# Optimization experiments

Measured on AMD Instinct MI355X. Metric: run time of the kernel, lower is better.

## Reference

```python
import jax, jax.numpy as jnp
import numpy as np

DIM = 1024
NUM_HEADS = 16
HEAD_DIM = DIM // NUM_HEADS
SCALE = HEAD_DIM ** -0.5
NEG = -1e9


def setup_inputs() -> dict:
    key = jax.random.key(0)
    ks = jax.random.split(key, 10)
    B, N, M, C = 8, 1024, 1024, DIM
    q = jax.random.normal(ks[0], (B, N, C), jnp.float32)
    k = jax.random.normal(ks[1], (B, M, C), jnp.float32)
    v = jax.random.normal(ks[2], (B, M, C), jnp.float32)
    mask = jax.random.randint(ks[3], (B, N), 0, 2, jnp.int32)
    target_mask = jax.random.randint(ks[4], (B, N, M), 0, 2, jnp.int32)
    Wq = jax.random.normal(ks[5], (C, C), jnp.float32) * 0.02
    Wk = jax.random.normal(ks[6], (C, C), jnp.float32) * 0.02
    Wv = jax.random.normal(ks[7], (C, C), jnp.float32) * 0.02
    Wo = jax.random.normal(ks[8], (C, C), jnp.float32) * 0.02
    bo = jnp.zeros((C,), jnp.float32)
    return {"q": q, "k": k, "v": v, "mask": mask, "target_mask": target_mask,
            "Wq": Wq, "Wk": Wk, "Wv": Wv, "Wo": Wo, "bo": bo}


def reference(q, k, v, mask, target_mask, Wq, Wk, Wv, Wo, bo):
    B, N, C = q.shape
    M = k.shape[1]
    H, D = NUM_HEADS, HEAD_DIM
    qh = (q @ Wq).reshape(B, N, H, D)
    kh = (k @ Wk).reshape(B, M, H, D)
    vh = (v @ Wv).reshape(B, M, H, D)
    attn = jnp.einsum('bnhd,bmhd->bhnm', qh, kh) * SCALE  # (B,H,N,M)
    # self-attn key mask (B,N) -> broadcast over queries (requires N==M as in original)
    attn = jnp.where(mask[:, None, None, :] == 0, NEG, attn)
    # cross-attn mask (B,N,M) -> broadcast over heads
    attn = jnp.where(target_mask[:, None, :, :] == 0, NEG, attn)
    attn = jax.nn.softmax(attn, axis=-1)
    x = jnp.einsum('bhnm,bmhd->bnhd', attn, vh).reshape(B, N, C)
    return x @ Wo + bo
```

## Files before the change

kernel.cpp:

```cpp
#include <hip/hip_runtime.h>
#include <hip/hip_bf16.h>

#define DEV __device__ __forceinline__

typedef __attribute__((ext_vector_type(8))) short bf16x8;
typedef __attribute__((ext_vector_type(4))) float f32x4;
typedef unsigned int u32;
typedef unsigned long long u64;

DEV short f2bf(float f) {
  union { float f; u32 u; } x; x.f = f;
  u32 r = x.u + 0x7fffu + ((x.u >> 16) & 1u);
  return (short)(r >> 16);
}

DEV void gload_lds16(const void* g, void* l) {
  __builtin_amdgcn_global_load_lds(
      (const __attribute__((address_space(1))) u32*)g,
      (__attribute__((address_space(3))) u32*)l, 16, 0, 0);
}

DEV void stage_t128(const char* base, int ktb, char* lds, int w, int lane) {
  int r8 = lane >> 3;
  int csw = ((lane & 7) ^ r8) << 4;
#pragma unroll
  for (int i = 0; i < 4; ++i) {
    int c = w * 4 + i;
    gload_lds16(base + (size_t)(c * 8 + r8) * 2048 + ktb + csw, lds + c * 1024);
  }
}

DEV bf16x8 frag(const short* L, int row, int col) {
  return *(const bf16x8*)&L[row * 64 + (col ^ ((row & 7) << 3))];
}

__global__ __launch_bounds__(256) void aconv(const float* __restrict__ q,
    const float* __restrict__ k, const float* __restrict__ v,
    short* __restrict__ qb, short* __restrict__ kb, short* __restrict__ vb) {
  const float* src; short* dst;
  if (blockIdx.z == 0)      { src = q; dst = qb; }
  else if (blockIdx.z == 1) { src = k; dst = kb; }
  else                      { src = v; dst = vb; }
  size_t i = ((size_t)blockIdx.x * 256 + threadIdx.x) * 8;
  float4 f0 = *(const float4*)(src + i);
  float4 f1 = *(const float4*)(src + i + 4);
  bf16x8 o;
  o[0] = f2bf(f0.x); o[1] = f2bf(f0.y); o[2] = f2bf(f0.z); o[3] = f2bf(f0.w);
  o[4] = f2bf(f1.x); o[5] = f2bf(f1.y); o[6] = f2bf(f1.z); o[7] = f2bf(f1.w);
  *(bf16x8*)(dst + i) = o;
}

__global__ __launch_bounds__(256) void pack_mask(const int* __restrict__ mask,
                                                 const int* __restrict__ tmask,
                                                 u64* __restrict__ pk) {
  int bn = blockIdx.x;
  int b = bn >> 10;
  int t = threadIdx.x, w = t >> 6, lane = t & 63;
  const int* tr = tmask + (size_t)bn * 1024;
  const int* mr = mask + b * 1024;
#pragma unroll
  for (int it = 0; it < 4; ++it) {
    int m = it * 256 + w * 64 + lane;
    bool on = (mr[m] != 0) && (tr[m] != 0);
    u64 bits = __ballot(on);
    if (lane == 0) pk[(size_t)bn * 16 + it * 4 + w] = bits;
  }
}

__global__ __launch_bounds__(256) void wconv4(const float* __restrict__ W0,
    const float* __restrict__ W1, const float* __restrict__ W2,
    const float* __restrict__ W3, short* __restrict__ WtAll) {
  const float* W = blockIdx.z == 0 ? W0 : blockIdx.z == 1 ? W1
                 : blockIdx.z == 2 ? W2 : W3;
  short* Wt = WtAll + (size_t)blockIdx.z * 1024 * 1024;
  __shared__ short tile[64][65];
  int k0 = blockIdx.x * 64, n0 = blockIdx.y * 64;
  int t = threadIdx.x;
  int r = t >> 2, c = (t & 3) * 16;
  const float* src = W + (size_t)(k0 + r) * 1024 + n0 + c;
#pragma unroll
  for (int i = 0; i < 16; i += 4) {
    float4 f = *(const float4*)(src + i);
    tile[r][c + i + 0] = f2bf(f.x);
    tile[r][c + i + 1] = f2bf(f.y);
    tile[r][c + i + 2] = f2bf(f.z);
    tile[r][c + i + 3] = f2bf(f.w);
  }
  __syncthreads();
  bf16x8 v0, v1;
#pragma unroll
  for (int i = 0; i < 8; ++i) v0[i] = tile[c + i][r];
#pragma unroll
  for (int i = 0; i < 8; ++i) v1[i] = tile[c + 8 + i][r];
  short* dst = Wt + (size_t)(n0 + r) * 1024 + k0 + c;
  *(bf16x8*)(dst) = v0;
  *(bf16x8*)(dst + 8) = v1;
}

__global__ __launch_bounds__(256) void vtrans(const short* __restrict__ vh,
                                              short* __restrict__ vht) {
  __shared__ short tile[64][65];
  int m0 = blockIdx.x * 64;
  int bh = blockIdx.y;
  int t = threadIdx.x;
  int r = t >> 2, c = (t & 3) * 16;
  const short* src = vh + ((size_t)bh * 1024 + m0 + r) * 64 + c;
  bf16x8 a0 = *(const bf16x8*)(src);
  bf16x8 a1 = *(const bf16x8*)(src + 8);
#pragma unroll
  for (int i = 0; i < 8; ++i) tile[r][c + i] = a0[i];
#pragma unroll
  for (int i = 0; i < 8; ++i) tile[r][c + 8 + i] = a1[i];
  __syncthreads();
  bf16x8 v0, v1;
#pragma unroll
  for (int i = 0; i < 8; ++i) v0[i] = tile[c + i][r];
#pragma unroll
  for (int i = 0; i < 8; ++i) v1[i] = tile[c + 8 + i][r];
  short* dst = vht + ((size_t)bh * 64 + r) * 1024 + m0 + c;
  *(bf16x8*)dst = v0;
  *(bf16x8*)(dst + 8) = v1;
}

#define QSCALE 0.18033688011112042f

__global__ __launch_bounds__(256, 2) void gemm_qkv(
    const short* __restrict__ qb, const short* __restrict__ kb, const short* __restrict__ vb,
    const short* __restrict__ WtAll,
    short* __restrict__ qh, short* __restrict__ kh, short* __restrict__ vh) {
  int flat = blockIdx.z * 512 + blockIdx.y * 8 + blockIdx.x;
  int nid = (flat & 7) * 192 + (flat >> 3);
  int zz = nid >> 9;
  int rr = nid & 511;
  int bm = (rr >> 3) * 128, bn = (rr & 7) * 128;

  const short* A; short* Ch; float cs;
  if (zz == 0)      { A = qb; Ch = qh; cs = QSCALE; }
  else if (zz == 1) { A = kb; Ch = kh; cs = 1.0f; }
  else              { A = vb; Ch = vh; cs = 1.0f; }
  const short* Wt = WtAll + (size_t)zz * 1024 * 1024;

  __shared__ __align__(16) short As[128 * 64];
  __shared__ __align__(16) short Bs[128 * 64];

  int tid = threadIdx.x;
  int lane = tid & 63, w = tid >> 6;
  int wm = w >> 1, wn = w & 1;
  int lr = lane & 15, lg = lane >> 4;

  const f32x4 fz = {0.f, 0.f, 0.f, 0.f};
  f32x4 acc[4][4];
#pragma unroll
  for (int i = 0; i < 4; ++i)
#pragma unroll
    for (int j = 0; j < 4; ++j) acc[i][j] = fz;

  const char* abase = (const char*)A + (size_t)bm * 2048;
  const char* bbase = (const char*)Wt + (size_t)bn * 2048;

  for (int ktb = 0; ktb < 2048; ktb += 128) {
    stage_t128(abase, ktb, (char*)As, w, lane);
    stage_t128(bbase, ktb, (char*)Bs, w, lane);
    __syncthreads();
#pragma unroll
    for (int ks = 0; ks < 2; ++ks) {
      bf16x8 af[4], bfr[4];
#pragma unroll
      for (int mi = 0; mi < 4; ++mi)
        af[mi] = frag(As, wm * 64 + mi * 16 + lr, ks * 32 + lg * 8);
#pragma unroll
      for (int ni = 0; ni < 4; ++ni)
        bfr[ni] = frag(Bs, wn * 64 + ni * 16 + lr, ks * 32 + lg * 8);
#pragma unroll
      for (int mi = 0; mi < 4; ++mi)
#pragma unroll
        for (int ni = 0; ni < 4; ++ni)
          acc[mi][ni] = __builtin_amdgcn_mfma_f32_16x16x32_bf16(af[mi], bfr[ni], acc[mi][ni], 0, 0, 0);
    }
    __syncthreads();
  }
#pragma unroll
  for (int mi = 0; mi < 4; ++mi)
#pragma unroll
    for (int ni = 0; ni < 4; ++ni) {
      int ccol = bn + wn * 64 + ni * 16 + lr;
      int h = ccol >> 6, d = ccol & 63;
#pragma unroll
      for (int j = 0; j < 4; ++j) {
        int r = bm + wm * 64 + mi * 16 + lg * 4 + j;
        int bb = r >> 10, n = r & 1023;
        Ch[(((size_t)bb * 16 + h) * 1024 + n) * 64 + d] = f2bf(acc[mi][ni][j] * cs);
      }
    }
}

DEV void stage_kv(const char* kbase, const char* vbase, int kv0,
                  short* Ksb, short* Vsb, int w, int lane) {
#pragma unroll
  for (int i = 0; i < 2; ++i) {
    int c = w * 2 + i;
    int row = (lane >> 3);
    int colb = ((lane & 7) ^ row) << 4;
    gload_lds16(kbase + (size_t)(kv0 + c * 8 + row) * 128 + colb, (char*)Ksb + c * 1024);
    gload_lds16(vbase + (size_t)(c * 8 + row) * 2048 + kv0 * 2 + colb, (char*)Vsb + c * 1024);
  }
}

__global__ __launch_bounds__(256, 2) void attn(
    const short* __restrict__ qh, const short* __restrict__ kh, const short* __restrict__ vht,
    const u64* __restrict__ pk, short* __restrict__ x) {
  __shared__ __align__(16) short Ks[2][4096];
  __shared__ __align__(16) short Vs[2][4096];
  __shared__ __align__(16) short Ps[2][8192];

  int flat = blockIdx.y * 8 + blockIdx.x;
  int nid = (flat & 7) * 64 + (flat >> 3);
  int bh = nid >> 2, qp = nid & 3;
  int b = bh >> 4;
  int tid = threadIdx.x, lane = tid & 63, w = tid >> 6;
  int lr = lane & 15, lg = lane >> 4;

  bf16x8 qa[2][2][2];
#pragma unroll
  for (int sub = 0; sub < 2; ++sub) {
    const short* qb2 = qh + ((size_t)bh * 1024 + qp * 256 + sub * 128 + w * 32) * 64;
#pragma unroll
    for (int mi = 0; mi < 2; ++mi)
#pragma unroll
      for (int ks = 0; ks < 2; ++ks)
        qa[sub][mi][ks] = *(const bf16x8*)(qb2 + (mi * 16 + lr) * 64 + ks * 32 + lg * 8);
  }

  const f32x4 fz = {0.f, 0.f, 0.f, 0.f};
  f32x4 o[2][2][4];
  float psum[2][2][4];
#pragma unroll
  for (int sub = 0; sub < 2; ++sub)
#pragma unroll
    for (int mi = 0; mi < 2; ++mi)
#pragma unroll
      for (int j = 0; j < 4; ++j) { psum[sub][mi][j] = 0.f; o[sub][mi][j] = fz; }

  const char* kbase = (const char*)(kh + (size_t)bh * 65536);
  const char* vbase = (const char*)(vht + (size_t)bh * 65536);
  const u64* pkb = pk + ((size_t)b * 1024 + qp * 256) * 16;

  stage_kv(kbase, vbase, 0, Ks[0], Vs[0], w, lane);
  __syncthreads();
  int cur = 0;

  for (int t = 0; t < 16; ++t) {
    if (t < 15) stage_kv(kbase, vbase, (t + 1) * 64, Ks[cur ^ 1], Vs[cur ^ 1], w, lane);

#pragma unroll
    for (int sub = 0; sub < 2; ++sub) {
      u64 pw[2][4];
#pragma unroll
      for (int mi = 0; mi < 2; ++mi)
#pragma unroll
        for (int j = 0; j < 4; ++j)
          pw[mi][j] = pkb[(sub * 128 + w * 32 + mi * 16 + lg * 4 + j) * 16 + t];

      f32x4 s[2][4];
#pragma unroll
      for (int mi = 0; mi < 2; ++mi)
#pragma unroll
        for (int ni = 0; ni < 4; ++ni) s[mi][ni] = fz;
      __builtin_amdgcn_s_setprio(1);
#pragma unroll
      for (int ks = 0; ks < 2; ++ks) {
        bf16x8 kb2[4];
#pragma unroll
        for (int ni = 0; ni < 4; ++ni)
          kb2[ni] = *(const bf16x8*)&Ks[cur][(ni * 16 + lr) * 64 + ((ks * 32 + lg * 8) ^ ((lr & 7) << 3))];
#pragma unroll
        for (int mi = 0; mi < 2; ++mi)
#pragma unroll
          for (int ni = 0; ni < 4; ++ni)
            s[mi][ni] = __builtin_amdgcn_mfma_f32_16x16x32_bf16(qa[sub][mi][ks], kb2[ni], s[mi][ni], 0, 0, 0);
      }
      __builtin_amdgcn_s_setprio(0);

#pragma unroll
      for (int mi = 0; mi < 2; ++mi)
#pragma unroll
        for (int j = 0; j < 4; ++j) {
          u32 lo = (u32)pw[mi][j], hi = (u32)(pw[mi][j] >> 32);
          int r = w * 32 + mi * 16 + lg * 4 + j;
          int sw = (r & 7) << 3;
          float rs = 0.f;
#pragma unroll
          for (int ni = 0; ni < 4; ++ni) {
            u32 bit = ((ni < 2 ? lo : hi) >> ((ni & 1) * 16 + lr)) & 1u;
            float e = __builtin_amdgcn_exp2f(s[mi][ni][j]);
            float p = bit ? e : 0.f;
            rs += p;
            union { float f; u32 u; } cv; cv.f = p;
            Ps[sub][r * 64 + ((ni * 16 + lr) ^ sw)] = (short)((cv.u + 0x8000u) >> 16);
          }
          psum[sub][mi][j] += rs;
        }

      __builtin_amdgcn_s_setprio(1);
#pragma unroll
      for (int ks = 0; ks < 2; ++ks) {
        bf16x8 pa[2], vb2[4];
#pragma unroll
        for (int mi = 0; mi < 2; ++mi)
          pa[mi] = *(const bf16x8*)&Ps[sub][(w * 32 + mi * 16 + lr) * 64 + ((ks * 32 + lg * 8) ^ ((lr & 7) << 3))];
#pragma unroll
        for (int nd = 0; nd < 4; ++nd)
          vb2[nd] = *(const bf16x8*)&Vs[cur][(nd * 16 + lr) * 64 + ((ks * 32 + lg * 8) ^ ((lr & 7) << 3))];
#pragma unroll
        for (int mi = 0; mi < 2; ++mi)
#pragma unroll
          for (int nd = 0; nd < 4; ++nd)
            o[sub][mi][nd] = __builtin_amdgcn_mfma_f32_16x16x32_bf16(pa[mi], vb2[nd], o[sub][mi][nd], 0, 0, 0);
      }
      __builtin_amdgcn_s_setprio(0);
    }
    __syncthreads();
    cur ^= 1;
  }

  short* xb = x + ((size_t)b * 1024) * 1024 + (bh & 15) * 64;
#pragma unroll
  for (int sub = 0; sub < 2; ++sub)
#pragma unroll
    for (int mi = 0; mi < 2; ++mi)
#pragma unroll
      for (int j = 0; j < 4; ++j) {
        float rs = psum[sub][mi][j];
#pragma unroll
        for (int dd = 1; dd < 16; dd <<= 1) rs += __shfl_xor(rs, dd, 64);
        float inv = rs > 0.f ? 1.0f / rs : 0.f;
        int qg = qp * 256 + sub * 128 + w * 32 + mi * 16 + lg * 4 + j;
#pragma unroll
        for (int nd = 0; nd < 4; ++nd) {
          int d = nd * 16 + lr;
          xb[(size_t)qg * 1024 + d] = f2bf(o[sub][mi][nd][j] * inv);
        }
      }
}

__global__ __launch_bounds__(256, 2) void gemm_out(
    const short* __restrict__ X, const short* __restrict__ Wot,
    const float* __restrict__ bo, float* __restrict__ out) {
  int flat = blockIdx.y * 8 + blockIdx.x;
  int nid = (flat & 7) * 64 + (flat >> 3);
  int bm = (nid >> 3) * 128, bn = (nid & 7) * 128;

  __shared__ __align__(16) short As[128 * 64];
  __shared__ __align__(16) short Bs[128 * 64];
  int tid = threadIdx.x, lane = tid & 63, w = tid >> 6;
  int wm = w >> 1, wn = w & 1, lr = lane & 15, lg = lane >> 4;

  const f32x4 fz = {0.f, 0.f, 0.f, 0.f};
  f32x4 acc[4][4];
#pragma unroll
  for (int i = 0; i < 4; ++i)
#pragma unroll
    for (int j = 0; j < 4; ++j) acc[i][j] = fz;

  const char* abase = (const char*)X + (size_t)bm * 2048;
  const char* bbase = (const char*)Wot + (size_t)bn * 2048;

  for (int ktb = 0; ktb < 2048; ktb += 128) {
    stage_t128(abase, ktb, (char*)As, w, lane);
    stage_t128(bbase, ktb, (char*)Bs, w, lane);
    __syncthreads();
#pragma unroll
    for (int ks = 0; ks < 2; ++ks) {
      bf16x8 af[4], bfr[4];
#pragma unroll
      for (int mi = 0; mi < 4; ++mi)
        af[mi] = frag(As, wm * 64 + mi * 16 + lr, ks * 32 + lg * 8);
#pragma unroll
      for (int ni = 0; ni < 4; ++ni)
        bfr[ni] = frag(Bs, wn * 64 + ni * 16 + lr, ks * 32 + lg * 8);
#pragma unroll
      for (int mi = 0; mi < 4; ++mi)
#pragma unroll
        for (int ni = 0; ni < 4; ++ni)
          acc[mi][ni] = __builtin_amdgcn_mfma_f32_16x16x32_bf16(af[mi], bfr[ni], acc[mi][ni], 0, 0, 0);
    }
    __syncthreads();
  }
#pragma unroll
  for (int mi = 0; mi < 4; ++mi)
#pragma unroll
    for (int ni = 0; ni < 4; ++ni) {
      int ccol = bn + wn * 64 + ni * 16 + lr;
      float bias = bo[ccol];
#pragma unroll
      for (int j = 0; j < 4; ++j) {
        int r = bm + wm * 64 + mi * 16 + lg * 4 + j;
        out[(size_t)r * 1024 + ccol] = acc[mi][ni][j] + bias;
      }
    }
}

extern "C" void kernel_launch(void* const* d_in, const int* in_sizes, int n_in,
                              void* d_out, int out_size, void* d_ws, size_t ws_size,
                              hipStream_t stream) {
  const float* q = (const float*)d_in[0];
  const float* k = (const float*)d_in[1];
  const float* v = (const float*)d_in[2];
  const int* mask = (const int*)d_in[3];
  const int* tmask = (const int*)d_in[4];
  const float* Wq = (const float*)d_in[5];
  const float* Wk = (const float*)d_in[6];
  const float* Wv = (const float*)d_in[7];
  const float* Wo = (const float*)d_in[8];
  const float* bo = (const float*)d_in[9];
  float* out = (float*)d_out;

  char* ws = (char*)d_ws;
  const size_t MB = 1u << 20;
  if (ws_size < 73 * MB) return;
  short* WtAll = (short*)(ws + 0 * MB);
  short* qh  = (short*)(ws + 8 * MB);
  short* kh  = (short*)(ws + 24 * MB);
  short* vh  = (short*)(ws + 40 * MB);
  short* vht = (short*)(ws + 56 * MB);
  u64*   pkb = (u64*)(ws + 72 * MB);
  short* x   = (short*)(ws + 40 * MB);
  short* qbA = (short*)d_out;
  short* kbA = (short*)d_out + 8 * 1024 * 1024;
  short* vbA = (short*)(ws + 56 * MB);

  aconv<<<dim3(4096, 1, 3), 256, 0, stream>>>(q, k, v, qbA, kbA, vbA);
  wconv4<<<dim3(16, 16, 4), 256, 0, stream>>>(Wq, Wk, Wv, Wo, WtAll);
  pack_mask<<<dim3(8192), 256, 0, stream>>>(mask, tmask, pkb);

  gemm_qkv<<<dim3(8, 64, 3), 256, 0, stream>>>(qbA, kbA, vbA, WtAll, qh, kh, vh);
  vtrans<<<dim3(16, 128), 256, 0, stream>>>(vh, vht);
  attn<<<dim3(8, 64), 256, 0, stream>>>(qh, kh, vht, pkb, x);
  gemm_out<<<dim3(8, 64), 256, 0, stream>>>(x, WtAll + 3 * 1024 * 1024, bo, out);
}
```

Baseline: 335.9 us.

## Triple-buffer GEMMs with 256x128 tiles and merge prologue kernels

Result: slower. 356.4 us (+6.1%).

```diff
diff --git a/kernel.cpp b/kernel.cpp
--- a/kernel.cpp
+++ b/kernel.cpp
@@ -8,6 +8,8 @@
 typedef unsigned int u32;
 typedef unsigned long long u64;
 
+#define VMCNT(n) asm volatile("s_waitcnt vmcnt(" #n ")" ::: "memory")
+
 DEV short f2bf(float f) {
   union { float f; u32 u; } x; x.f = f;
   u32 r = x.u + 0x7fffu + ((x.u >> 16) & 1u);
@@ -20,81 +22,123 @@
       (__attribute__((address_space(3))) u32*)l, 16, 0, 0);
 }
 
-DEV void stage_t128(const char* base, int ktb, char* lds, int w, int lane) {
+DEV bf16x8 frag(const short* L, int row, int col) {
+  return *(const bf16x8*)&L[row * 64 + (col ^ ((row & 7) << 3))];
+}
+
+DEV void stageA256(const char* base, int ktb, char* lds, int w, int lane) {
   int r8 = lane >> 3;
   int csw = ((lane & 7) ^ r8) << 4;
 #pragma unroll
-  for (int i = 0; i < 4; ++i) {
-    int c = w * 4 + i;
+  for (int l = 0; l < 4; ++l) {
+    int c = l * 8 + w;
     gload_lds16(base + (size_t)(c * 8 + r8) * 2048 + ktb + csw, lds + c * 1024);
   }
 }
-
-DEV bf16x8 frag(const short* L, int row, int col) {
-  return *(const bf16x8*)&L[row * 64 + (col ^ ((row & 7) << 3))];
-}
-
-__global__ __launch_bounds__(256) void aconv(const float* __restrict__ q,
-    const float* __restrict__ k, const float* __restrict__ v,
-    short* __restrict__ qb, short* __restrict__ kb, short* __restrict__ vb) {
-  const float* src; short* dst;
-  if (blockIdx.z == 0)      { src = q; dst = qb; }
-  else if (blockIdx.z == 1) { src = k; dst = kb; }
-  else                      { src = v; dst = vb; }
-  size_t i = ((size_t)blockIdx.x * 256 + threadIdx.x) * 8;
-  float4 f0 = *(const float4*)(src + i);
-  float4 f1 = *(const float4*)(src + i + 4);
-  bf16x8 o;
-  o[0] = f2bf(f0.x); o[1] = f2bf(f0.y); o[2] = f2bf(f0.z); o[3] = f2bf(f0.w);
-  o[4] = f2bf(f1.x); o[5] = f2bf(f1.y); o[6] = f2bf(f1.z); o[7] = f2bf(f1.w);
-  *(bf16x8*)(dst + i) = o;
-}
-
-__global__ __launch_bounds__(256) void pack_mask(const int* __restrict__ mask,
-                                                 const int* __restrict__ tmask,
-                                                 u64* __restrict__ pk) {
-  int bn = blockIdx.x;
-  int b = bn >> 10;
-  int t = threadIdx.x, w = t >> 6, lane = t & 63;
-  const int* tr = tmask + (size_t)bn * 1024;
-  const int* mr = mask + b * 1024;
-#pragma unroll
-  for (int it = 0; it < 4; ++it) {
-    int m = it * 256 + w * 64 + lane;
-    bool on = (mr[m] != 0) && (tr[m] != 0);
-    u64 bits = __ballot(on);
-    if (lane == 0) pk[(size_t)bn * 16 + it * 4 + w] = bits;
-  }
-}
-
-__global__ __launch_bounds__(256) void wconv4(const float* __restrict__ W0,
-    const float* __restrict__ W1, const float* __restrict__ W2,
-    const float* __restrict__ W3, short* __restrict__ WtAll) {
-  const float* W = blockIdx.z == 0 ? W0 : blockIdx.z == 1 ? W1
-                 : blockIdx.z == 2 ? W2 : W3;
-  short* Wt = WtAll + (size_t)blockIdx.z * 1024 * 1024;
-  __shared__ short tile[64][65];
-  int k0 = blockIdx.x * 64, n0 = blockIdx.y * 64;
-  int t = threadIdx.x;
-  int r = t >> 2, c = (t & 3) * 16;
-  const float* src = W + (size_t)(k0 + r) * 1024 + n0 + c;
-#pragma unroll
-  for (int i = 0; i < 16; i += 4) {
-    float4 f = *(const float4*)(src + i);
-    tile[r][c + i + 0] = f2bf(f.x);
-    tile[r][c + i + 1] = f2bf(f.y);
-    tile[r][c + i + 2] = f2bf(f.z);
-    tile[r][c + i + 3] = f2bf(f.w);
-  }
-  __syncthreads();
-  bf16x8 v0, v1;
-#pragma unroll
-  for (int i = 0; i < 8; ++i) v0[i] = tile[c + i][r];
-#pragma unroll
-  for (int i = 0; i < 8; ++i) v1[i] = tile[c + 8 + i][r];
-  short* dst = Wt + (size_t)(n0 + r) * 1024 + k0 + c;
-  *(bf16x8*)(dst) = v0;
-  *(bf16x8*)(dst + 8) = v1;
+DEV void stageB128(const char* base, int ktb, char* lds, int w, int lane) {
+  int r8 = lane >> 3;
+  int csw = ((lane & 7) ^ r8) << 4;
+#pragma unroll
+  for (int l = 0; l < 2; ++l) {
+    int c = l * 8 + w;
+    gload_lds16(base + (size_t)(c * 8 + r8) * 2048 + ktb + csw, lds + c * 1024);
+  }
+}
+
+DEV void tile_compute(const short* Asb, const short* Bsb, f32x4 acc[8][2],
+                      int wm, int wn, int lr, int lg) {
+  bf16x8 bfrag[2][2];
+#pragma unroll
+  for (int ni = 0; ni < 2; ++ni)
+#pragma unroll
+    for (int ks = 0; ks < 2; ++ks)
+      bfrag[ni][ks] = frag(Bsb, wn * 32 + ni * 16 + lr, ks * 32 + lg * 8);
+#pragma unroll
+  for (int pi = 0; pi < 4; ++pi) {
+    bf16x8 af[2][2];
+#pragma unroll
+    for (int m2 = 0; m2 < 2; ++m2)
+#pragma unroll
+      for (int ks = 0; ks < 2; ++ks)
+        af[m2][ks] = frag(Asb, wm * 128 + (pi * 2 + m2) * 16 + lr, ks * 32 + lg * 8);
+    __builtin_amdgcn_s_setprio(1);
+#pragma unroll
+    for (int m2 = 0; m2 < 2; ++m2)
+#pragma unroll
+      for (int ni = 0; ni < 2; ++ni)
+#pragma unroll
+        for (int ks = 0; ks < 2; ++ks)
+          acc[pi * 2 + m2][ni] = __builtin_amdgcn_mfma_f32_16x16x32_bf16(
+              af[m2][ks], bfrag[ni][ks], acc[pi * 2 + m2][ni], 0, 0, 0);
+    __builtin_amdgcn_s_setprio(0);
+  }
+}
+
+#define ENTRY_SYNC()                          \
+  __builtin_amdgcn_sched_barrier(0);          \
+  __builtin_amdgcn_s_barrier();               \
+  __builtin_amdgcn_sched_barrier(0)
+
+__global__ __launch_bounds__(256) void prologue(
+    const float* __restrict__ q, const float* __restrict__ k, const float* __restrict__ v,
+    short* __restrict__ qb, short* __restrict__ kb, short* __restrict__ vb,
+    const float* __restrict__ W0, const float* __restrict__ W1,
+    const float* __restrict__ W2, const float* __restrict__ W3,
+    short* __restrict__ WtAll,
+    const int* __restrict__ mask, const int* __restrict__ tmask, u64* __restrict__ pk) {
+  int bx = blockIdx.x;
+  if (bx < 12288) {
+    int z = bx >> 12, bi = bx & 4095;
+    const float* src = z == 0 ? q : z == 1 ? k : v;
+    short* dst = z == 0 ? qb : z == 1 ? kb : vb;
+    size_t i = ((size_t)bi * 256 + threadIdx.x) * 8;
+    float4 f0 = *(const float4*)(src + i);
+    float4 f1 = *(const float4*)(src + i + 4);
+    bf16x8 o;
+    o[0] = f2bf(f0.x); o[1] = f2bf(f0.y); o[2] = f2bf(f0.z); o[3] = f2bf(f0.w);
+    o[4] = f2bf(f1.x); o[5] = f2bf(f1.y); o[6] = f2bf(f1.z); o[7] = f2bf(f1.w);
+    *(bf16x8*)(dst + i) = o;
+  } else if (bx < 13312) {
+    int idx = bx - 12288;
+    int z = idx >> 8, rem = idx & 255;
+    const float* W = z == 0 ? W0 : z == 1 ? W1 : z == 2 ? W2 : W3;
+    short* Wt = WtAll + (size_t)z * 1024 * 1024;
+    __shared__ short tile[64][65];
+    int k0 = (rem >> 4) * 64, n0 = (rem & 15) * 64;
+    int t = threadIdx.x;
+    int r = t >> 2, c = (t & 3) * 16;
+    const float* src = W + (size_t)(k0 + r) * 1024 + n0 + c;
+#pragma unroll
+    for (int i = 0; i < 16; i += 4) {
+      float4 f = *(const float4*)(src + i);
+      tile[r][c + i + 0] = f2bf(f.x);
+      tile[r][c + i + 1] = f2bf(f.y);
+      tile[r][c + i + 2] = f2bf(f.z);
+      tile[r][c + i + 3] = f2bf(f.w);
+    }
+    __syncthreads();
+    bf16x8 v0, v1;
+#pragma unroll
+    for (int i = 0; i < 8; ++i) v0[i] = tile[c + i][r];
+#pragma unroll
+    for (int i = 0; i < 8; ++i) v1[i] = tile[c + 8 + i][r];
+    short* dst = Wt + (size_t)(n0 + r) * 1024 + k0 + c;
+    *(bf16x8*)(dst) = v0;
+    *(bf16x8*)(dst + 8) = v1;
+  } else {
+    int bn = bx - 13312;
+    int b = bn >> 10;
+    int t = threadIdx.x, w = t >> 6, lane = t & 63;
+    const int* tr = tmask + (size_t)bn * 1024;
+    const int* mr = mask + b * 1024;
+#pragma unroll
+    for (int it = 0; it < 4; ++it) {
+      int m = it * 256 + w * 64 + lane;
+      bool on = (mr[m] != 0) && (tr[m] != 0);
+      u64 bits = __ballot(on);
+      if (lane == 0) pk[(size_t)bn * 16 + it * 4 + w] = bits;
+    }
+  }
 }
 
 __global__ __launch_bounds__(256) void vtrans(const short* __restrict__ vh,
@@ -124,15 +168,18 @@
 
 #define QSCALE 0.18033688011112042f
 
-__global__ __launch_bounds__(256, 2) void gemm_qkv(
+__global__ __launch_bounds__(512, 2) void gemm_qkv(
     const short* __restrict__ qb, const short* __restrict__ kb, const short* __restrict__ vb,
     const short* __restrict__ WtAll,
     short* __restrict__ qh, short* __restrict__ kh, short* __restrict__ vh) {
-  int flat = blockIdx.z * 512 + blockIdx.y * 8 + blockIdx.x;
-  int nid = (flat & 7) * 192 + (flat >> 3);
-  int zz = nid >> 9;
-  int rr = nid & 511;
-  int bm = (rr >> 3) * 128, bn = (rr & 7) * 128;
+  __shared__ __align__(16) short AsAll[3 * 256 * 64];
+  __shared__ __align__(16) short BsAll[3 * 128 * 64];
+
+  int flat = blockIdx.y * 8 + blockIdx.x;
+  int nid = (flat & 7) * 96 + (flat >> 3);
+  int zz = nid >> 8;
+  int rr = nid & 255;
+  int bm = (rr >> 3) * 256, bn = (rr & 7) * 128;
 
   const short* A; short* Ch; float cs;
   if (zz == 0)      { A = qb; Ch = qh; cs = QSCALE; }
@@ -140,56 +187,109 @@
   else              { A = vb; Ch = vh; cs = 1.0f; }
   const short* Wt = WtAll + (size_t)zz * 1024 * 1024;
 
-  __shared__ __align__(16) short As[128 * 64];
-  __shared__ __align__(16) short Bs[128 * 64];
-
   int tid = threadIdx.x;
   int lane = tid & 63, w = tid >> 6;
-  int wm = w >> 1, wn = w & 1;
+  int wm = w >> 2, wn = w & 3;
   int lr = lane & 15, lg = lane >> 4;
 
   const f32x4 fz = {0.f, 0.f, 0.f, 0.f};
-  f32x4 acc[4][4];
-#pragma unroll
-  for (int i = 0; i < 4; ++i)
-#pragma unroll
-    for (int j = 0; j < 4; ++j) acc[i][j] = fz;
+  f32x4 acc[8][2];
+#pragma unroll
+  for (int i = 0; i < 8; ++i) { acc[i][0] = fz; acc[i][1] = fz; }
 
   const char* abase = (const char*)A + (size_t)bm * 2048;
   const char* bbase = (const char*)Wt + (size_t)bn * 2048;
 
-  for (int ktb = 0; ktb < 2048; ktb += 128) {
-    stage_t128(abase, ktb, (char*)As, w, lane);
-    stage_t128(bbase, ktb, (char*)Bs, w, lane);
-    __syncthreads();
-#pragma unroll
-    for (int ks = 0; ks < 2; ++ks) {
-      bf16x8 af[4], bfr[4];
-#pragma unroll
-      for (int mi = 0; mi < 4; ++mi)
-        af[mi] = frag(As, wm * 64 + mi * 16 + lr, ks * 32 + lg * 8);
-#pragma unroll
-      for (int ni = 0; ni < 4; ++ni)
-        bfr[ni] = frag(Bs, wn * 64 + ni * 16 + lr, ks * 32 + lg * 8);
-#pragma unroll
-      for (int mi = 0; mi < 4; ++mi)
-#pragma unroll
-        for (int ni = 0; ni < 4; ++ni)
-          acc[mi][ni] = __builtin_amdgcn_mfma_f32_16x16x32_bf16(af[mi], bfr[ni], acc[mi][ni], 0, 0, 0);
-    }
-    __syncthreads();
-  }
-#pragma unroll
-  for (int mi = 0; mi < 4; ++mi)
-#pragma unroll
-    for (int ni = 0; ni < 4; ++ni) {
-      int ccol = bn + wn * 64 + ni * 16 + lr;
+  stageA256(abase, 0, (char*)AsAll, w, lane);
+  stageB128(bbase, 0, (char*)BsAll, w, lane);
+  stageA256(abase, 128, (char*)AsAll + 32768, w, lane);
+  stageB128(bbase, 128, (char*)BsAll + 16384, w, lane);
+
+  int cb = 0, sb = 2;
+  for (int t = 0; t < 15; ++t) {
+    VMCNT(6);
+    ENTRY_SYNC();
+    if (t < 14) {
+      stageA256(abase, (t + 2) * 128, (char*)AsAll + sb * 32768, w, lane);
+      stageB128(bbase, (t + 2) * 128, (char*)BsAll + sb * 16384, w, lane);
+    }
+    tile_compute(AsAll + cb * 16384, BsAll + cb * 8192, acc, wm, wn, lr, lg);
+    cb = (cb == 2) ? 0 : cb + 1;
+    sb = (sb == 2) ? 0 : sb + 1;
+  }
+  VMCNT(0);
+  ENTRY_SYNC();
+  tile_compute(AsAll + cb * 16384, BsAll + cb * 8192, acc, wm, wn, lr, lg);
+
+#pragma unroll
+  for (int mi = 0; mi < 8; ++mi)
+#pragma unroll
+    for (int ni = 0; ni < 2; ++ni) {
+      int ccol = bn + wn * 32 + ni * 16 + lr;
       int h = ccol >> 6, d = ccol & 63;
 #pragma unroll
       for (int j = 0; j < 4; ++j) {
-        int r = bm + wm * 64 + mi * 16 + lg * 4 + j;
+        int r = bm + wm * 128 + mi * 16 + lg * 4 + j;
         int bb = r >> 10, n = r & 1023;
         Ch[(((size_t)bb * 16 + h) * 1024 + n) * 64 + d] = f2bf(acc[mi][ni][j] * cs);
+      }
+    }
+}
+
+__global__ __launch_bounds__(512, 2) void gemm_out(
+    const short* __restrict__ X, const short* __restrict__ Wot,
+    const float* __restrict__ bo, float* __restrict__ out) {
+  __shared__ __align__(16) short AsAll[3 * 256 * 64];
+  __shared__ __align__(16) short BsAll[3 * 128 * 64];
+
+  int flat = blockIdx.y * 8 + blockIdx.x;
+  int nid = (flat & 7) * 32 + (flat >> 3);
+  int bm = (nid >> 3) * 256, bn = (nid & 7) * 128;
+
+  int tid = threadIdx.x;
+  int lane = tid & 63, w = tid >> 6;
+  int wm = w >> 2, wn = w & 3;
+  int lr = lane & 15, lg = lane >> 4;
+
+  const f32x4 fz = {0.f, 0.f, 0.f, 0.f};
+  f32x4 acc[8][2];
+#pragma unroll
+  for (int i = 0; i < 8; ++i) { acc[i][0] = fz; acc[i][1] = fz; }
+
+  const char* abase = (const char*)X + (size_t)bm * 2048;
+  const char* bbase = (const char*)Wot + (size_t)bn * 2048;
+
+  stageA256(abase, 0, (char*)AsAll, w, lane);
+  stageB128(bbase, 0, (char*)BsAll, w, lane);
+  stageA256(abase, 128, (char*)AsAll + 32768, w, lane);
+  stageB128(bbase, 128, (char*)BsAll + 16384, w, lane);
+
+  int cb = 0, sb = 2;
+  for (int t = 0; t < 15; ++t) {
+    VMCNT(6);
+    ENTRY_SYNC();
+    if (t < 14) {
+      stageA256(abase, (t + 2) * 128, (char*)AsAll + sb * 32768, w, lane);
+      stageB128(bbase, (t + 2) * 128, (char*)BsAll + sb * 16384, w, lane);
+    }
+    tile_compute(AsAll + cb * 16384, BsAll + cb * 8192, acc, wm, wn, lr, lg);
+    cb = (cb == 2) ? 0 : cb + 1;
+    sb = (sb == 2) ? 0 : sb + 1;
+  }
+  VMCNT(0);
+  ENTRY_SYNC();
+  tile_compute(AsAll + cb * 16384, BsAll + cb * 8192, acc, wm, wn, lr, lg);
+
+#pragma unroll
+  for (int mi = 0; mi < 8; ++mi)
+#pragma unroll
+    for (int ni = 0; ni < 2; ++ni) {
+      int ccol = bn + wn * 32 + ni * 16 + lr;
+      float bias = bo[ccol];
+#pragma unroll
+      for (int j = 0; j < 4; ++j) {
+        int r = bm + wm * 128 + mi * 16 + lg * 4 + j;
+        out[(size_t)r * 1024 + ccol] = acc[mi][ni][j] + bias;
       }
     }
 }
@@ -341,63 +441,6 @@
           xb[(size_t)qg * 1024 + d] = f2bf(o[sub][mi][nd][j] * inv);
         }
       }
-}
-
-__global__ __launch_bounds__(256, 2) void gemm_out(
-    const short* __restrict__ X, const short* __restrict__ Wot,
-    const float* __restrict__ bo, float* __restrict__ out) {
-  int flat = blockIdx.y * 8 + blockIdx.x;
-  int nid = (flat & 7) * 64 + (flat >> 3);
-  int bm = (nid >> 3) * 128, bn = (nid & 7) * 128;
-
-  __shared__ __align__(16) short As[128 * 64];
-  __shared__ __align__(16) short Bs[128 * 64];
-  int tid = threadIdx.x, lane = tid & 63, w = tid >> 6;
-  int wm = w >> 1, wn = w & 1, lr = lane & 15, lg = lane >> 4;
-
-  const f32x4 fz = {0.f, 0.f, 0.f, 0.f};
-  f32x4 acc[4][4];
-#pragma unroll
-  for (int i = 0; i < 4; ++i)
-#pragma unroll
-    for (int j = 0; j < 4; ++j) acc[i][j] = fz;
-
-  const char* abase = (const char*)X + (size_t)bm * 2048;
-  const char* bbase = (const char*)Wot + (size_t)bn * 2048;
-
-  for (int ktb = 0; ktb < 2048; ktb += 128) {
-    stage_t128(abase, ktb, (char*)As, w, lane);
-    stage_t128(bbase, ktb, (char*)Bs, w, lane);
-    __syncthreads();
-#pragma unroll
-    for (int ks = 0; ks < 2; ++ks) {
-      bf16x8 af[4], bfr[4];
-#pragma unroll
-      for (int mi = 0; mi < 4; ++mi)
-        af[mi] = frag(As, wm * 64 + mi * 16 + lr, ks * 32 + lg * 8);
-#pragma unroll
-      for (int ni = 0; ni < 4; ++ni)
-        bfr[ni] = frag(Bs, wn * 64 + ni * 16 + lr, ks * 32 + lg * 8);
-#pragma unroll
-      for (int mi = 0; mi < 4; ++mi)
-#pragma unroll
-        for (int ni = 0; ni < 4; ++ni)
-          acc[mi][ni] = __builtin_amdgcn_mfma_f32_16x16x32_bf16(af[mi], bfr[ni], acc[mi][ni], 0, 0, 0);
-    }
-    __syncthreads();
-  }
-#pragma unroll
-  for (int mi = 0; mi < 4; ++mi)
-#pragma unroll
-    for (int ni = 0; ni < 4; ++ni) {
-      int ccol = bn + wn * 64 + ni * 16 + lr;
-      float bias = bo[ccol];
-#pragma unroll
-      for (int j = 0; j < 4; ++j) {
-        int r = bm + wm * 64 + mi * 16 + lg * 4 + j;
-        out[(size_t)r * 1024 + ccol] = acc[mi][ni][j] + bias;
-      }
-    }
 }
 
 extern "C" void kernel_launch(void* const* d_in, const int* in_sizes, int n_in,
@@ -429,12 +472,11 @@
   short* kbA = (short*)d_out + 8 * 1024 * 1024;
   short* vbA = (short*)(ws + 56 * MB);
 
-  aconv<<<dim3(4096, 1, 3), 256, 0, stream>>>(q, k, v, qbA, kbA, vbA);
-  wconv4<<<dim3(16, 16, 4), 256, 0, stream>>>(Wq, Wk, Wv, Wo, WtAll);
-  pack_mask<<<dim3(8192), 256, 0, stream>>>(mask, tmask, pkb);
-
-  gemm_qkv<<<dim3(8, 64, 3), 256, 0, stream>>>(qbA, kbA, vbA, WtAll, qh, kh, vh);
+  prologue<<<dim3(21504), 256, 0, stream>>>(q, k, v, qbA, kbA, vbA,
+                                            Wq, Wk, Wv, Wo, WtAll,
+                                            mask, tmask, pkb);
+  gemm_qkv<<<dim3(8, 96), 512, 0, stream>>>(qbA, kbA, vbA, WtAll, qh, kh, vh);
   vtrans<<<dim3(16, 128), 256, 0, stream>>>(vh, vht);
   attn<<<dim3(8, 64), 256, 0, stream>>>(qh, kh, vht, pkb, x);
-  gemm_out<<<dim3(8, 64), 256, 0, stream>>>(x, WtAll + 3 * 1024 * 1024, bo, out);
-}
+  gemm_out<<<dim3(8, 32), 512, 0, stream>>>(x, WtAll + 3 * 1024 * 1024, bo, out);
+}
```
